# Optimization experiments

Hardware: AMD Instinct MI355X
Metric: run time of the kernel (lower is better)

## Reference

```python
import jax, jax.numpy as jnp
import numpy as np

SMPL_PARENT = np.array([0,0,0,1,2,3,4,5,6,7,8,9,9,9,12,13,14,16,17,18,19,20,21], dtype=np.int64)

def quat2mat(quat):
    # quat: [N,4] (w,x,y,z) -> [N,3,3]
    q = quat / jnp.linalg.norm(quat, axis=1, keepdims=True)
    w, x, y, z = q[:, 0], q[:, 1], q[:, 2], q[:, 3]
    w2, x2, y2, z2 = w*w, x*x, y*y, z*z
    wx, wy, wz = w*x, w*y, w*z
    xy, xz, yz = x*y, x*z, y*z
    R = jnp.stack([w2+x2-y2-z2, 2*xy-2*wz, 2*wy+2*xz,
                   2*wz+2*xy, w2-x2+y2-z2, 2*yz-2*wx,
                   2*xz-2*wy, 2*wx+2*yz, w2-x2-y2+z2], axis=1)
    return R.reshape(-1, 3, 3)

def rodrigues(theta):
    # theta: [N,3] axis-angle -> [N,3,3]
    angle = jnp.linalg.norm(theta + 1e-8, axis=1, keepdims=True)
    normalized = theta / angle
    half = angle * 0.5
    quat = jnp.concatenate([jnp.cos(half), jnp.sin(half) * normalized], axis=1)
    return quat2mat(quat)

def setup_inputs() -> dict:
    key = jax.random.key(0)
    ks = jax.random.split(key, 8)
    B, V = 64, 50000
    pose = jax.random.normal(ks[0], (B, 72), dtype=jnp.float32) * 0.3
    beta = jax.random.normal(ks[1], (B, 300), dtype=jnp.float32) * 0.03
    v_template = jax.random.normal(ks[2], (V, 3), dtype=jnp.float32)
    shapedirs = jax.random.normal(ks[3], (V, 3, 300), dtype=jnp.float32) * 0.01
    posedirs = jax.random.normal(ks[4], (V, 3, 207), dtype=jnp.float32) * 0.01
    Jr = jax.random.uniform(ks[5], (24, V), dtype=jnp.float32)
    J_regressor = Jr / jnp.sum(Jr, axis=1, keepdims=True)
    w = jax.random.uniform(ks[6], (V, 24), dtype=jnp.float32)
    weights = w / jnp.sum(w, axis=1, keepdims=True)
    parent = jnp.asarray(SMPL_PARENT)
    return {"pose": pose, "beta": beta, "v_template": v_template,
            "shapedirs": shapedirs, "posedirs": posedirs,
            "J_regressor": J_regressor, "weights": weights, "parent": parent}

def reference(pose, beta, v_template, shapedirs, posedirs, J_regressor, weights, parent):
    B = pose.shape[0]
    parent_np = np.asarray(jax.device_get(parent))
    # shape blendshapes: [B,V,3]
    v_shaped = jnp.einsum('vds,bs->bvd', shapedirs, beta) + v_template[None]
    J = jnp.einsum('jv,bvd->bjd', J_regressor, v_shaped)
    # pose -> rotation matrices [B,24,3,3]
    R = rodrigues(pose.reshape(-1, 3)).reshape(B, 24, 3, 3)
    lrotmin = (R[:, 1:] - jnp.eye(3, dtype=R.dtype)).reshape(B, 207)
    # pose blendshapes
    v_posed = v_shaped + jnp.einsum('vdp,bp->bvd', posedirs, lrotmin)
    # relative joint locations
    J_rel = J.at[:, 1:].set(J[:, 1:] - J[:, parent_np])
    # local transforms [B,24,4,4]
    G_top = jnp.concatenate([R, J_rel[..., None]], axis=-1)  # [B,24,3,4]
    pad = jnp.broadcast_to(jnp.array([0., 0., 0., 1.], dtype=R.dtype), (B, 24, 1, 4))
    G_local = jnp.concatenate([G_top, pad], axis=2)
    # kinematic chain (24 structurally-distinct joints)
    Gs = [G_local[:, 0]]
    for i in range(1, 24):
        Gs.append(jnp.matmul(Gs[parent_np[i - 1]], G_local[:, i]))
    G = jnp.stack(Gs, axis=1)  # [B,24,4,4]
    # remove rest-pose translation: G[...,:,3] -= G @ [J,0]
    rest4 = jnp.concatenate([J, jnp.zeros((B, 24, 1), dtype=J.dtype)], axis=2)  # [B,24,4]
    corr = jnp.einsum('bjmn,bjn->bjm', G, rest4)
    G = G.at[..., :, 3].add(-corr)
    # LBS: per-vertex transform [B,V,4,4]
    T = jnp.einsum('vj,bjmn->bvmn', weights, G)
    v_h = jnp.concatenate([v_posed, jnp.ones_like(v_posed[..., :1])], axis=-1)  # [B,V,4]
    v = jnp.einsum('bvmn,bvn->bvm', T, v_h)[..., :3]
    return v
```

## Files before the change

kernel.cpp:

```cpp
#include <hip/hip_runtime.h>
#include <math.h>

#define NV 50000
#define NM 150000

__constant__ int c_par[24]   = {0, 0,0,0, 1,2,3, 4,5,6, 7,8,9,9,9, 12,13,14, 16,17, 18,19, 20,21};
__constant__ int c_depth[24] = {0, 1,1,1, 2,2,2, 3,3,3, 4,4,4,4,4, 5,5,5, 6,6, 7,7, 8,8};

__global__ __launch_bounds__(256)
void prep_kernel(const float* __restrict__ beta, float* __restrict__ betaT,
                 float* __restrict__ J)
{
    int i = blockIdx.x * 256 + threadIdx.x;
    if (i < 300 * 64) {
        int k = i >> 6, b = i & 63;
        betaT[i] = beta[b * 300 + k];
    }
    if (i < 64 * 24 * 3) J[i] = 0.f;
}

template<int K, int MODE>
__global__ __launch_bounds__(128)
void gemm_kernel(const float* __restrict__ A, const float* __restrict__ Bt,
                 const float* __restrict__ add, float* __restrict__ C)
{
    __shared__ float As[64 * 33];
    const int t    = threadIdx.x;
    const int row0 = blockIdx.x * 64;
    const int lrow = t & 63;
    const int half = __builtin_amdgcn_readfirstlane(t >> 6);
    const int row  = row0 + lrow;

    float acc[32];
    #pragma unroll
    for (int b = 0; b < 32; ++b) acc[b] = 0.f;

    const int srow = t >> 3;
    const int skg  = t & 7;

    const int nfull = K / 32;
    for (int c = 0; c < nfull; ++c) {
        const int k0 = c * 32;
        __syncthreads();
        #pragma unroll
        for (int p = 0; p < 4; ++p) {
            int r = p * 16 + srow;
            float4 v = make_float4(0.f, 0.f, 0.f, 0.f);
            if (row0 + r < NM)
                v = *(const float4*)(A + (size_t)(row0 + r) * K + k0 + skg * 4);
            float* d = As + r * 33 + skg * 4;
            d[0] = v.x; d[1] = v.y; d[2] = v.z; d[3] = v.w;
        }
        __syncthreads();
        #pragma unroll 4
        for (int k = 0; k < 32; ++k) {
            float a = As[lrow * 33 + k];
            const float* Bk = Bt + (size_t)(k0 + k) * 64 + half * 32;
            #pragma unroll
            for (int b = 0; b < 32; ++b) acc[b] = fmaf(Bk[b], a, acc[b]);
        }
    }
    const int krem = K - nfull * 32;
    if (krem > 0) {
        const int k0 = nfull * 32;
        __syncthreads();
        #pragma unroll
        for (int p = 0; p < 4; ++p) {
            int r = p * 16 + srow;
            #pragma unroll
            for (int q = 0; q < 4; ++q) {
                int k = skg * 4 + q;
                float v = 0.f;
                if (k < krem && row0 + r < NM)
                    v = A[(size_t)(row0 + r) * K + k0 + k];
                As[r * 33 + k] = v;
            }
        }
        __syncthreads();
        for (int k = 0; k < krem; ++k) {
            float a = As[lrow * 33 + k];
            const float* Bk = Bt + (size_t)(k0 + k) * 64 + half * 32;
            #pragma unroll
            for (int b = 0; b < 32; ++b) acc[b] = fmaf(Bk[b], a, acc[b]);
        }
    }

    if (row >= NM) return;
    if constexpr (MODE == 0) {
        float t0 = add[row];
        float* dst = C + (size_t)row * 64 + half * 32;
        #pragma unroll
        for (int q = 0; q < 8; ++q) {
            float4 v = {acc[q*4+0] + t0, acc[q*4+1] + t0, acc[q*4+2] + t0, acc[q*4+3] + t0};
            *(float4*)(dst + q * 4) = v;
        }
    } else {
        const float* av = add + (size_t)row * 64 + half * 32;
        #pragma unroll
        for (int b = 0; b < 32; ++b)
            C[(size_t)(half * 32 + b) * NM + row] = acc[b] + av[b];
    }
}

__global__ __launch_bounds__(256)
void jreduce_kernel(const float* __restrict__ vs, const float* __restrict__ Jr,
                    float* J)
{
    const int tid = threadIdx.x;
    const int b = tid & 63;
    const int g = __builtin_amdgcn_readfirstlane(tid >> 6);
    float acc[6][3];
    #pragma unroll
    for (int jj = 0; jj < 6; ++jj) { acc[jj][0]=0.f; acc[jj][1]=0.f; acc[jj][2]=0.f; }
    const int v0 = blockIdx.x * 250;
    for (int v = v0; v < v0 + 250; ++v) {
        float p0 = vs[(size_t)(v*3+0)*64 + b];
        float p1 = vs[(size_t)(v*3+1)*64 + b];
        float p2 = vs[(size_t)(v*3+2)*64 + b];
        #pragma unroll
        for (int jj = 0; jj < 6; ++jj) {
            float r = Jr[(size_t)(g*6+jj)*NV + v];
            acc[jj][0] += r*p0; acc[jj][1] += r*p1; acc[jj][2] += r*p2;
        }
    }
    #pragma unroll
    for (int jj = 0; jj < 6; ++jj)
        #pragma unroll
        for (int d = 0; d < 3; ++d)
            atomicAdd(&J[(size_t)(b*24 + g*6 + jj)*3 + d], acc[jj][d]);
}

__global__ __launch_bounds__(192)
void pose_kernel(const float* __restrict__ pose, const float* __restrict__ J,
                 float* __restrict__ G, float* __restrict__ lrotT)
{
    __shared__ float Gl[8][24][12];
    __shared__ float Gc[8][24][12];
    const int t  = threadIdx.x;
    const int bl = t / 24;
    const int j  = t % 24;
    const int b  = blockIdx.x * 8 + bl;

    float tx = pose[b*72 + j*3 + 0];
    float ty = pose[b*72 + j*3 + 1];
    float tz = pose[b*72 + j*3 + 2];
    float ax = tx + 1e-8f, ay = ty + 1e-8f, az = tz + 1e-8f;
    float angle = sqrtf(ax*ax + ay*ay + az*az);
    float nx = tx / angle, ny = ty / angle, nz = tz / angle;
    float half = 0.5f * angle;
    float sw = sinf(half);
    float qw = cosf(half), qx = sw*nx, qy = sw*ny, qz = sw*nz;
    float qn = sqrtf(qw*qw + qx*qx + qy*qy + qz*qz);
    qw /= qn; qx /= qn; qy /= qn; qz /= qn;
    float w2=qw*qw, x2=qx*qx, y2=qy*qy, z2=qz*qz;
    float xy=qx*qy, xz=qx*qz, yz=qy*qz, wx=qw*qx, wy=qw*qy, wz=qw*qz;
    float r00 = w2+x2-y2-z2, r01 = 2.f*(xy-wz), r02 = 2.f*(wy+xz);
    float r10 = 2.f*(wz+xy), r11 = w2-x2+y2-z2, r12 = 2.f*(yz-wx);
    float r20 = 2.f*(xz-wy), r21 = 2.f*(wx+yz), r22 = w2-x2-y2+z2;

    if (j >= 1) {
        const int k9 = (j-1)*9;
        lrotT[(size_t)(k9+0)*64+b]=r00-1.f; lrotT[(size_t)(k9+1)*64+b]=r01;
        lrotT[(size_t)(k9+2)*64+b]=r02;     lrotT[(size_t)(k9+3)*64+b]=r10;
        lrotT[(size_t)(k9+4)*64+b]=r11-1.f; lrotT[(size_t)(k9+5)*64+b]=r12;
        lrotT[(size_t)(k9+6)*64+b]=r20;     lrotT[(size_t)(k9+7)*64+b]=r21;
        lrotT[(size_t)(k9+8)*64+b]=r22-1.f;
    }
    float jx = J[(size_t)(b*24+j)*3+0];
    float jy = J[(size_t)(b*24+j)*3+1];
    float jz = J[(size_t)(b*24+j)*3+2];
    float rx = jx, ry = jy, rz = jz;
    if (j > 0) {
        int p = c_par[j];
        rx -= J[(size_t)(b*24+p)*3+0];
        ry -= J[(size_t)(b*24+p)*3+1];
        rz -= J[(size_t)(b*24+p)*3+2];
    }
    float* gl = Gl[bl][j];
    gl[0]=r00; gl[1]=r01; gl[2]=r02;  gl[3]=rx;
    gl[4]=r10; gl[5]=r11; gl[6]=r12;  gl[7]=ry;
    gl[8]=r20; gl[9]=r21; gl[10]=r22; gl[11]=rz;
    __syncthreads();

    if (j == 0) {
        #pragma unroll
        for (int c = 0; c < 12; ++c) Gc[bl][0][c] = Gl[bl][0][c];
    }
    const int dj = c_depth[j];
    for (int lvl = 1; lvl <= 8; ++lvl) {
        __syncthreads();
        if (dj == lvl) {
            const float* Aa = Gc[bl][c_par[j]];
            const float* Bb = Gl[bl][j];
            float* D = Gc[bl][j];
            #pragma unroll
            for (int r = 0; r < 3; ++r) {
                float a0=Aa[r*4+0], a1=Aa[r*4+1], a2=Aa[r*4+2], a3=Aa[r*4+3];
                D[r*4+0] = a0*Bb[0] + a1*Bb[4] + a2*Bb[8];
                D[r*4+1] = a0*Bb[1] + a1*Bb[5] + a2*Bb[9];
                D[r*4+2] = a0*Bb[2] + a1*Bb[6] + a2*Bb[10];
                D[r*4+3] = a0*Bb[3] + a1*Bb[7] + a2*Bb[11] + a3;
            }
        }
    }
    __syncthreads();

    const float* Gi = Gc[bl][j];
    float* go = G + (size_t)(b*24 + j) * 12;
    #pragma unroll
    for (int r = 0; r < 3; ++r) {
        go[r*4+0] = Gi[r*4+0];
        go[r*4+1] = Gi[r*4+1];
        go[r*4+2] = Gi[r*4+2];
        go[r*4+3] = Gi[r*4+3] - (Gi[r*4+0]*jx + Gi[r*4+1]*jy + Gi[r*4+2]*jz);
    }
}

__global__ __launch_bounds__(256)
void skin_kernel(const float* __restrict__ vp, const float* __restrict__ G,
                 const float* __restrict__ wts, float* __restrict__ out)
{
    const int v = blockIdx.x * 256 + threadIdx.x;
    if (v >= NV) return;
    const int b0 = blockIdx.y * 8;
    float w[24];
    const float4* wp = (const float4*)(wts + (size_t)v * 24);
    #pragma unroll
    for (int q = 0; q < 6; ++q) {
        float4 t = wp[q];
        w[q*4+0]=t.x; w[q*4+1]=t.y; w[q*4+2]=t.z; w[q*4+3]=t.w;
    }
    for (int b = b0; b < b0 + 8; ++b) {
        const float* pb = vp + (size_t)b * NM + v*3;
        float px = pb[0], py = pb[1], pz = pb[2];
        float ox = 0.f, oy = 0.f, oz = 0.f;
        const float* Gb = G + (size_t)b * 24 * 12;
        #pragma unroll
        for (int j = 0; j < 24; ++j) {
            const float* g = Gb + j*12;
            float wj = w[j];
            ox += wj * (g[0]*px + g[1]*py + g[2]*pz  + g[3]);
            oy += wj * (g[4]*px + g[5]*py + g[6]*pz  + g[7]);
            oz += wj * (g[8]*px + g[9]*py + g[10]*pz + g[11]);
        }
        float* ob = out + (size_t)b * NM + v*3;
        ob[0] = ox; ob[1] = oy; ob[2] = oz;
    }
}

extern "C" void kernel_launch(void* const* d_in, const int* in_sizes, int n_in,
                              void* d_out, int out_size, void* d_ws, size_t ws_size,
                              hipStream_t stream) {
    const float* pose       = (const float*)d_in[0];
    const float* beta       = (const float*)d_in[1];
    const float* v_template = (const float*)d_in[2];
    const float* shapedirs  = (const float*)d_in[3];
    const float* posedirs   = (const float*)d_in[4];
    const float* Jreg       = (const float*)d_in[5];
    const float* weights    = (const float*)d_in[6];
    float* out = (float*)d_out;

    char* ws = (char*)d_ws;
    float* vs_ws    = (float*)(ws);
    float* vp_ws    = (float*)(ws + 38400000);
    float* betaT_ws = (float*)(ws + 38400000);
    float* J_ws     = (float*)(ws + 76800000);
    float* G_ws     = (float*)(ws + 76818432);
    float* lrotT_ws = (float*)(ws + 76892160);

    prep_kernel<<<75, 256, 0, stream>>>(beta, betaT_ws, J_ws);
    gemm_kernel<300, 0><<<2344, 128, 0, stream>>>(shapedirs, betaT_ws, v_template, vs_ws);
    jreduce_kernel<<<200, 256, 0, stream>>>(vs_ws, Jreg, J_ws);
    pose_kernel<<<8, 192, 0, stream>>>(pose, J_ws, G_ws, lrotT_ws);
    gemm_kernel<207, 1><<<2344, 128, 0, stream>>>(posedirs, lrotT_ws, vs_ws, vp_ws);
    skin_kernel<<<dim3(196, 8), 256, 0, stream>>>(vp_ws, G_ws, weights, out);
}
```

Before: 709.4 us.

## Restructure joint regression: per-wave vertex split with LDS block reduction

The joint-regression kernel now gives each wave all 24 joints over its own slice of 25 vertices, instead of splitting joints across waves. Each vertex's shaped-position load is then shared by all joints, and the 8 waves' partial sums are combined in shared memory before one atomic per output per block. The goal is to cut redundant global reads and the number of global atomics. The cost is 72 accumulators per thread, which adds register pressure and may lower occupancy.

```diff
diff --git a/kernel.cpp b/kernel.cpp
--- a/kernel.cpp
+++ b/kernel.cpp
@@ -102,32 +102,56 @@
     }
 }
 
-__global__ __launch_bounds__(256)
+__global__ __launch_bounds__(512)
 void jreduce_kernel(const float* __restrict__ vs, const float* __restrict__ Jr,
                     float* J)
 {
-    const int tid = threadIdx.x;
-    const int b = tid & 63;
-    const int g = __builtin_amdgcn_readfirstlane(tid >> 6);
-    float acc[6][3];
-    #pragma unroll
-    for (int jj = 0; jj < 6; ++jj) { acc[jj][0]=0.f; acc[jj][1]=0.f; acc[jj][2]=0.f; }
-    const int v0 = blockIdx.x * 250;
-    for (int v = v0; v < v0 + 250; ++v) {
+    __shared__ float Ls[4][64][73];
+    const int t = threadIdx.x;
+    const int b = t & 63;
+    const int w = __builtin_amdgcn_readfirstlane(t >> 6);
+
+    float acc[24][3];
+    #pragma unroll
+    for (int j = 0; j < 24; ++j) { acc[j][0]=0.f; acc[j][1]=0.f; acc[j][2]=0.f; }
+
+    const int v0 = blockIdx.x * 200 + w * 25;
+    #pragma unroll 5
+    for (int v = v0; v < v0 + 25; ++v) {
         float p0 = vs[(size_t)(v*3+0)*64 + b];
         float p1 = vs[(size_t)(v*3+1)*64 + b];
         float p2 = vs[(size_t)(v*3+2)*64 + b];
         #pragma unroll
-        for (int jj = 0; jj < 6; ++jj) {
-            float r = Jr[(size_t)(g*6+jj)*NV + v];
-            acc[jj][0] += r*p0; acc[jj][1] += r*p1; acc[jj][2] += r*p2;
-        }
-    }
-    #pragma unroll
-    for (int jj = 0; jj < 6; ++jj)
-        #pragma unroll
-        for (int d = 0; d < 3; ++d)
-            atomicAdd(&J[(size_t)(b*24 + g*6 + jj)*3 + d], acc[jj][d]);
+        for (int j = 0; j < 24; ++j) {
+            float r = Jr[(size_t)j*NV + v];
+            acc[j][0] += r*p0; acc[j][1] += r*p1; acc[j][2] += r*p2;
+        }
+    }
+
+    if (w < 4) {
+        float* d = Ls[w][b];
+        #pragma unroll
+        for (int j = 0; j < 24; ++j) {
+            d[j*3+0] = acc[j][0]; d[j*3+1] = acc[j][1]; d[j*3+2] = acc[j][2];
+        }
+    }
+    __syncthreads();
+    if (w >= 4) {
+        float* d = Ls[w-4][b];
+        #pragma unroll
+        for (int j = 0; j < 24; ++j) {
+            d[j*3+0] += acc[j][0]; d[j*3+1] += acc[j][1]; d[j*3+2] += acc[j][2];
+        }
+    }
+    __syncthreads();
+
+    #pragma unroll
+    for (int q = 0; q < 9; ++q) {
+        int oid = t * 9 + q;
+        int bb = oid / 72, c = oid - bb * 72;
+        float s = Ls[0][bb][c] + Ls[1][bb][c] + Ls[2][bb][c] + Ls[3][bb][c];
+        atomicAdd(&J[(size_t)bb * 72 + c], s);
+    }
 }
 
 __global__ __launch_bounds__(192)
@@ -270,7 +294,7 @@
 
     prep_kernel<<<75, 256, 0, stream>>>(beta, betaT_ws, J_ws);
     gemm_kernel<300, 0><<<2344, 128, 0, stream>>>(shapedirs, betaT_ws, v_template, vs_ws);
-    jreduce_kernel<<<200, 256, 0, stream>>>(vs_ws, Jreg, J_ws);
+    jreduce_kernel<<<250, 512, 0, stream>>>(vs_ws, Jreg, J_ws);
     pose_kernel<<<8, 192, 0, stream>>>(pose, J_ws, G_ws, lrotT_ws);
     gemm_kernel<207, 1><<<2344, 128, 0, stream>>>(posedirs, lrotT_ws, vs_ws, vp_ws);
     skin_kernel<<<dim3(196, 8), 256, 0, stream>>>(vp_ws, G_ws, weights, out);
```

Measured after the change: 628.4 us. 1.13x faster.
